# Kernel tuning notes

Measured on AMD Instinct MI355X. Metric: run time of the kernel, lower is better.

Reference implementation:

```python
import jax, jax.numpy as jnp
import numpy as np

B, DIM, H, W = 2, 256, 32, 32
HALF, DI, DS, DTR = DIM // 2, 256, 16, 8
DEPTH, K1 = 2, 4


def _ln(x, w, b, eps=1e-5):
    m = jnp.mean(x, -1, keepdims=True)
    v = jnp.var(x, -1, keepdims=True)
    return (x - m) * jax.lax.rsqrt(v + eps) * w + b


def _selective_scan(dA, dBu, C):
    # dA, dBu: (N, L, D, S); C: (N, L, S) -> y: (N, L, D)
    def step(h, ab):
        a, b = ab
        h = a * h + b
        return h, h
    h0 = jnp.zeros((dA.shape[0],) + dA.shape[2:], dA.dtype)
    _, hs = jax.lax.scan(step, h0, (jnp.moveaxis(dA, 1, 0), jnp.moveaxis(dBu, 1, 0)))
    return jnp.einsum('lnds,nls->nld', hs, C)


def _mamba_block(xs, ln_w, ln_b, in_w, cw, cb, xw, dtw, dtb, Alog, Dp, ow):
    # xs: (B, L, HALF); canonical Mamba-1 block, pre-LN residual
    Lq = xs.shape[1]
    h = _ln(xs, ln_w, ln_b)
    u, z = jnp.split(h @ in_w, 2, axis=-1)  # (B,L,DI) each
    up = jnp.pad(u, ((0, 0), (K1 - 1, 0), (0, 0)))  # causal depthwise conv1d
    u = sum(up[:, k:k + Lq, :] * cw[:, k] for k in range(K1)) + cb
    u = jax.nn.silu(u)
    dbc = u @ xw
    dtr, Bm, Cm = jnp.split(dbc, [DTR, DTR + DS], axis=-1)
    dt = jax.nn.softplus(dtr @ dtw + dtb)  # (B,L,DI)
    A = -jnp.exp(Alog)  # (DI,DS)
    dA = jnp.exp(dt[..., None] * A)
    dBu = (dt * u)[..., None] * Bm[:, :, None, :]
    y = _selective_scan(dA, dBu, Cm) + u * Dp
    return xs + (y * jax.nn.silu(z)) @ ow


def _vss_block(x, ln_w, ln_b, in_w, cw, cb, xw, dtw, dtb, Alog, Dp, on_w, on_b, ow):
    # x: (B, HALF, H, W); VMamba SS2D block (4-direction cross-scan), pre-LN residual
    Bq, _, Hq, Wq = x.shape
    Lq = Hq * Wq
    h = _ln(x.transpose(0, 2, 3, 1), ln_w, ln_b)
    u, z = jnp.split(h @ in_w, 2, axis=-1)  # (B,H,W,DI)
    u2 = jax.lax.conv_general_dilated(u.transpose(0, 3, 1, 2), cw[:, None], (1, 1), ((1, 1), (1, 1)),
                                      feature_group_count=DI,
                                      dimension_numbers=('NCHW', 'OIHW', 'NCHW')) + cb[None, :, None, None]
    u2 = jax.nn.silu(u2)  # (B,DI,H,W)
    s0 = u2.reshape(Bq, DI, Lq)
    s1 = u2.transpose(0, 1, 3, 2).reshape(Bq, DI, Lq)
    us = jnp.stack([s0, s1, jnp.flip(s0, -1), jnp.flip(s1, -1)], 1).transpose(0, 1, 3, 2)  # (B,4,L,DI)
    dbc = jnp.einsum('bkld,kdr->bklr', us, xw)
    dtr, Bm, Cm = jnp.split(dbc, [DTR, DTR + DS], axis=-1)
    dt = jax.nn.softplus(jnp.einsum('bklr,krd->bkld', dtr, dtw) + dtb[None, :, None, :])
    A = -jnp.exp(Alog)  # (4,DI,DS)
    dA = jnp.exp(dt[..., None] * A[None, :, None])  # (B,4,L,DI,DS)
    dBu = (dt * us)[..., None] * Bm[:, :, :, None, :]
    y = _selective_scan(dA.reshape(Bq * 4, Lq, DI, DS), dBu.reshape(Bq * 4, Lq, DI, DS), Cm.reshape(Bq * 4, Lq, DS))
    y = y.reshape(Bq, 4, Lq, DI) + us * Dp[None, :, None, :]
    yt = y.transpose(0, 1, 3, 2)  # (B,4,DI,L)
    y0 = yt[:, 0]
    y1 = yt[:, 1].reshape(Bq, DI, Wq, Hq).transpose(0, 1, 3, 2).reshape(Bq, DI, Lq)
    y2 = jnp.flip(yt[:, 2], -1)
    y3 = jnp.flip(yt[:, 3], -1).reshape(Bq, DI, Wq, Hq).transpose(0, 1, 3, 2).reshape(Bq, DI, Lq)
    ym = _ln((y0 + y1 + y2 + y3).transpose(0, 2, 1), on_w, on_b)  # (B,L,DI)
    out = (ym * jax.nn.silu(z.reshape(Bq, Lq, DI))) @ ow  # (B,L,HALF)
    return x + out.reshape(Bq, Hq, Wq, HALF).transpose(0, 3, 1, 2)


def _fwd(x, proj1_w, proj1_b, proj2_w, proj2_b,
         m_ln_w, m_ln_b, m_in_w, m_conv_w, m_conv_b, m_xproj_w, m_dt_w, m_dt_b, m_Alog, m_D, m_out_w,
         v_ln_w, v_ln_b, v_in_w, v_conv_w, v_conv_b, v_xproj_w, v_dt_w, v_dt_b, v_Alog, v_D,
         v_onorm_w, v_onorm_b, v_out_w, fuse_w, fuse_b, bn_g, bn_b, bn_m, bn_v):
    Bq, _, Hq, Wq = x.shape
    Lq = Hq * Wq
    p1 = jnp.einsum('oc,bchw->bohw', proj1_w, x) + proj1_b[None, :, None, None]
    s = p1.reshape(Bq, HALF, Lq).transpose(0, 2, 1)
    for i in range(DEPTH):
        s = _mamba_block(s, m_ln_w[i], m_ln_b[i], m_in_w[i], m_conv_w[i], m_conv_b[i], m_xproj_w[i],
                         m_dt_w[i], m_dt_b[i], m_Alog[i], m_D[i], m_out_w[i])
    p1 = s.transpose(0, 2, 1).reshape(Bq, HALF, Hq, Wq)
    p2 = jnp.einsum('oc,bchw->bohw', proj2_w, x) + proj2_b[None, :, None, None]
    for i in range(DEPTH):
        p2 = _vss_block(p2, v_ln_w[i], v_ln_b[i], v_in_w[i], v_conv_w[i], v_conv_b[i], v_xproj_w[i],
                        v_dt_w[i], v_dt_b[i], v_Alog[i], v_D[i], v_onorm_w[i], v_onorm_b[i], v_out_w[i])
    xc = jnp.concatenate([p1, p2], 1)
    y = jax.lax.conv_general_dilated(xc, fuse_w, (1, 1), ((1, 1), (1, 1)),
                                     dimension_numbers=('NCHW', 'OIHW', 'NCHW')) + fuse_b[None, :, None, None]
    y = (y - bn_m[None, :, None, None]) * jax.lax.rsqrt(bn_v + 1e-5)[None, :, None, None] * bn_g[None, :, None, None] + bn_b[None, :, None, None]
    return jax.nn.relu(y)


def setup_inputs() -> dict:
    key = jax.random.key(0)
    ks = iter(jax.random.split(key, 64))
    n = lambda shape, s=0.02: jax.random.normal(next(ks), shape, jnp.float32) * s
    A_row = jnp.log(jnp.arange(1, DS + 1, dtype=jnp.float32))  # standard S4D-real init
    return {
        'x': jax.random.normal(next(ks), (B, DIM, H, W), jnp.float32),
        'proj1_w': n((HALF, DIM), 0.05), 'proj1_b': n((HALF,)),
        'proj2_w': n((HALF, DIM), 0.05), 'proj2_b': n((HALF,)),
        'm_ln_w': jnp.ones((DEPTH, HALF)), 'm_ln_b': jnp.zeros((DEPTH, HALF)),
        'm_in_w': n((DEPTH, HALF, 2 * DI)),
        'm_conv_w': n((DEPTH, DI, K1), 0.1), 'm_conv_b': n((DEPTH, DI)),
        'm_xproj_w': n((DEPTH, DI, DTR + 2 * DS)),
        'm_dt_w': n((DEPTH, DTR, DI), 0.1), 'm_dt_b': n((DEPTH, DI)),
        'm_Alog': jnp.array(jnp.broadcast_to(A_row, (DEPTH, DI, DS))),
        'm_D': jnp.ones((DEPTH, DI)),
        'm_out_w': n((DEPTH, DI, HALF)),
        'v_ln_w': jnp.ones((DEPTH, HALF)), 'v_ln_b': jnp.zeros((DEPTH, HALF)),
        'v_in_w': n((DEPTH, HALF, 2 * DI)),
        'v_conv_w': n((DEPTH, DI, 3, 3), 0.1), 'v_conv_b': n((DEPTH, DI)),
        'v_xproj_w': n((DEPTH, 4, DI, DTR + 2 * DS)),
        'v_dt_w': n((DEPTH, 4, DTR, DI), 0.1), 'v_dt_b': n((DEPTH, 4, DI)),
        'v_Alog': jnp.array(jnp.broadcast_to(A_row, (DEPTH, 4, DI, DS))),
        'v_D': jnp.ones((DEPTH, 4, DI)),
        'v_onorm_w': jnp.ones((DEPTH, DI)), 'v_onorm_b': jnp.zeros((DEPTH, DI)),
        'v_out_w': n((DEPTH, DI, HALF)),
        'fuse_w': n((DIM, DIM, 3, 3), 0.02), 'fuse_b': n((DIM,)),
        'bn_g': jnp.ones((DIM,)), 'bn_b': jnp.zeros((DIM,)),
        'bn_m': n((DIM,)), 'bn_v': jax.random.uniform(next(ks), (DIM,), jnp.float32, 0.5, 1.5),
    }


def reference(x, proj1_w, proj1_b, proj2_w, proj2_b,
              m_ln_w, m_ln_b, m_in_w, m_conv_w, m_conv_b, m_xproj_w, m_dt_w, m_dt_b, m_Alog, m_D, m_out_w,
              v_ln_w, v_ln_b, v_in_w, v_conv_w, v_conv_b, v_xproj_w, v_dt_w, v_dt_b, v_Alog, v_D,
              v_onorm_w, v_onorm_b, v_out_w, fuse_w, fuse_b, bn_g, bn_b, bn_m, bn_v):
    return _fwd(x, proj1_w, proj1_b, proj2_w, proj2_b,
                m_ln_w, m_ln_b, m_in_w, m_conv_w, m_conv_b, m_xproj_w, m_dt_w, m_dt_b, m_Alog, m_D, m_out_w,
                v_ln_w, v_ln_b, v_in_w, v_conv_w, v_conv_b, v_xproj_w, v_dt_w, v_dt_b, v_Alog, v_D,
                v_onorm_w, v_onorm_b, v_out_w, fuse_w, fuse_b, bn_g, bn_b, bn_m, bn_v)
```

## Files before the change

kernel.cpp:

```cpp
#include <hip/hip_runtime.h>
#include <math.h>

#define CH  16
#define NCH 64

typedef __attribute__((ext_vector_type(8))) short bf16x8;
typedef __attribute__((ext_vector_type(4))) float f32x4;
typedef __attribute__((ext_vector_type(4))) unsigned int u32x4;

__device__ __forceinline__ float dev_silu(float x){ return x * (1.0f/(1.0f + __expf(-x))); }
__device__ __forceinline__ float dev_softplus(float x){ return fmaxf(x,0.0f) + log1pf(__expf(-fabsf(x))); }
__device__ __forceinline__ unsigned short dev_bf16(float f){
    unsigned int u = __float_as_uint(f);
    return (unsigned short)((u + 0x7fffu + ((u >> 16) & 1u)) >> 16);
}

__global__ void __launch_bounds__(256)
k_wt(const float* __restrict__ w1, const float* __restrict__ w2, float* __restrict__ wtc)
{
    int bc = blockIdx.x;
    int ot = bc & 7, ct = bc >> 3;
    __shared__ float t[32][33];
    int col = threadIdx.x & 31, r8 = threadIdx.x >> 5;
    #pragma unroll
    for (int i = 0; i < 4; ++i){
        int r = i*8 + r8;
        int o = ot*32 + r;
        const float* src = (o < 128) ? (w1 + (size_t)o*256) : (w2 + (size_t)(o-128)*256);
        t[r][col] = src[ct*32 + col];
    }
    __syncthreads();
    #pragma unroll
    for (int i = 0; i < 4; ++i){
        int r = i*8 + r8;
        int c = ct*32 + r, o = ot*32 + col;
        wtc[(size_t)c*256 + o] = t[col][r];
    }
}

__global__ void __launch_bounds__(256)
k_proj(const float* __restrict__ x, const float* __restrict__ wtc,
       const float* __restrict__ b1, const float* __restrict__ b2,
       float* __restrict__ sm, float* __restrict__ sv)
{
    int blk = blockIdx.x;
    int b = blk >> 8, l0 = (blk & 255) * 4;
    int tid = threadIdx.x;
    __shared__ float4 xs[256];
    xs[tid] = *(const float4*)(x + ((size_t)(b*256 + tid))*1024 + l0);
    __syncthreads();
    int o = tid & 127;
    float bias = (tid < 128) ? b1[o] : b2[o];
    float a0 = bias, a1 = bias, a2 = bias, a3 = bias;
    #pragma unroll 4
    for (int c = 0; c < 256; ++c){
        float wv = wtc[(size_t)c*256 + tid];
        float4 xv = xs[c];
        a0 = fmaf(wv, xv.x, a0);
        a1 = fmaf(wv, xv.y, a1);
        a2 = fmaf(wv, xv.z, a2);
        a3 = fmaf(wv, xv.w, a3);
    }
    float* dst = (tid < 128) ? sm : sv;
    size_t base = ((size_t)b*1024 + l0)*128 + o;
    dst[base      ] = a0;
    dst[base + 128] = a1;
    dst[base + 256] = a2;
    dst[base + 384] = a3;
}

__global__ void __launch_bounds__(256)
k_lnmm(const float* __restrict__ s, const float* __restrict__ lnw, const float* __restrict__ lnb,
       const float* __restrict__ inw, float* __restrict__ u, float* __restrict__ z)
{
    int bl0 = blockIdx.x * 8;
    int tid = threadIdx.x;
    int row = tid >> 5, lane = tid & 31;
    __shared__ float hn[8][132];
    float4 v = *(const float4*)(s + (size_t)(bl0 + row)*128 + lane*4);
    float a = v.x + v.y + v.z + v.w;
    float q = v.x*v.x + v.y*v.y + v.z*v.z + v.w*v.w;
    #pragma unroll
    for (int o = 16; o; o >>= 1){ a += __shfl_xor(a, o); q += __shfl_xor(q, o); }
    float mean = a * (1.0f/128.0f);
    float rs = rsqrtf(q * (1.0f/128.0f) - mean*mean + 1e-5f);
    float4 w4 = *(const float4*)(lnw + lane*4);
    float4 b4 = *(const float4*)(lnb + lane*4);
    float4 hv;
    hv.x = (v.x-mean)*rs*w4.x + b4.x;
    hv.y = (v.y-mean)*rs*w4.y + b4.y;
    hv.z = (v.z-mean)*rs*w4.z + b4.z;
    hv.w = (v.w-mean)*rs*w4.w + b4.w;
    *(float4*)&hn[row][lane*4] = hv;
    __syncthreads();
    float acc0[8] = {0,0,0,0,0,0,0,0};
    float acc1[8] = {0,0,0,0,0,0,0,0};
    for (int c = 0; c < 128; c += 4){
        float w0[4], w1[4];
        #pragma unroll
        for (int i = 0; i < 4; ++i){
            w0[i] = inw[(size_t)(c+i)*512 + tid];
            w1[i] = inw[(size_t)(c+i)*512 + tid + 256];
        }
        #pragma unroll
        for (int r = 0; r < 8; ++r){
            float4 h4 = *(const float4*)&hn[r][c];
            acc0[r] = fmaf(h4.x, w0[0], acc0[r]);
            acc0[r] = fmaf(h4.y, w0[1], acc0[r]);
            acc0[r] = fmaf(h4.z, w0[2], acc0[r]);
            acc0[r] = fmaf(h4.w, w0[3], acc0[r]);
            acc1[r] = fmaf(h4.x, w1[0], acc1[r]);
            acc1[r] = fmaf(h4.y, w1[1], acc1[r]);
            acc1[r] = fmaf(h4.z, w1[2], acc1[r]);
            acc1[r] = fmaf(h4.w, w1[3], acc1[r]);
        }
    }
    #pragma unroll
    for (int r = 0; r < 8; ++r){
        u[(size_t)(bl0 + r)*256 + tid] = acc0[r];
        z[(size_t)(bl0 + r)*256 + tid] = acc1[r];
    }
}

__global__ void __launch_bounds__(256)
k_mconv(const float* __restrict__ ur, const float* __restrict__ cw, const float* __restrict__ cb,
        float* __restrict__ uc)
{
    int bl = blockIdx.x; int b = bl >> 10, l = bl & 1023; int d = threadIdx.x;
    float acc = cb[d];
    #pragma unroll
    for (int k = 0; k < 4; ++k){
        int lp = l - 3 + k;
        if (lp >= 0) acc = fmaf(ur[((size_t)(b<<10) + lp)*256 + d], cw[d*4 + k], acc);
    }
    uc[(size_t)bl*256 + d] = dev_silu(acc);
}

__global__ void __launch_bounds__(256)
k_vconv(const float* __restrict__ ur, const float* __restrict__ cw, const float* __restrict__ cb,
        float* __restrict__ us)
{
    int bl = blockIdx.x; int b = bl >> 10, l = bl & 1023; int d = threadIdx.x;
    int h = l >> 5, w = l & 31;
    float acc = cb[d];
    #pragma unroll
    for (int kh = 0; kh < 3; ++kh){
        int hh = h + kh - 1; if (hh < 0 || hh > 31) continue;
        #pragma unroll
        for (int kw = 0; kw < 3; ++kw){
            int ww = w + kw - 1; if (ww < 0 || ww > 31) continue;
            acc = fmaf(ur[((size_t)(b<<10) + (hh<<5) + ww)*256 + d], cw[d*9 + kh*3 + kw], acc);
        }
    }
    float v = dev_silu(acc);
    int l1 = (w<<5) + h;
    size_t base = (size_t)b*4*1024*256;
    us[base + ((size_t)0*1024 + l        )*256 + d] = v;
    us[base + ((size_t)1*1024 + l1       )*256 + d] = v;
    us[base + ((size_t)2*1024 + (1023-l ))*256 + d] = v;
    us[base + ((size_t)3*1024 + (1023-l1))*256 + d] = v;
}

__global__ void __launch_bounds__(256)
k_xproj(const float* __restrict__ u, const float* __restrict__ xw, const float* __restrict__ dtw,
        const float* __restrict__ dtb, float* __restrict__ dt, float* __restrict__ Bm,
        float* __restrict__ Cm, int K)
{
    int blk = blockIdx.x;
    int bk = blk >> 8; int k = bk % K;
    int l0 = (blk & 255) * 4;
    size_t idx0 = (size_t)bk*1024 + l0;
    int tid = threadIdx.x;
    __shared__ float ursh[4][256];
    __shared__ float dbc[4][44];
    #pragma unroll
    for (int p = 0; p < 4; ++p)
        ursh[p][tid] = u[(idx0 + p)*256 + tid];
    __syncthreads();
    if (tid < 160){
        int r = tid % 40, p = tid / 40;
        const float* xwc = xw + (size_t)k*256*40 + r;
        float a0 = 0.f, a1 = 0.f;
        for (int c = 0; c < 128; ++c){
            a0 = fmaf(ursh[p][c],       xwc[(size_t)c*40],       a0);
            a1 = fmaf(ursh[p][c + 128], xwc[(size_t)(c+128)*40], a1);
        }
        dbc[p][r] = a0 + a1;
    }
    __syncthreads();
    const float* dtwk = dtw + (size_t)k*8*256;
    float bias = dtb[k*256 + tid];
    float wv[8];
    #pragma unroll
    for (int r = 0; r < 8; ++r) wv[r] = dtwk[r*256 + tid];
    #pragma unroll
    for (int p = 0; p < 4; ++p){
        float a = bias;
        #pragma unroll
        for (int r = 0; r < 8; ++r) a = fmaf(dbc[p][r], wv[r], a);
        dt[(idx0 + p)*256 + tid] = dev_softplus(a);
    }
    if (tid < 128){
        int p = tid >> 5, j = tid & 31;
        if (j < 16) Bm[(idx0 + p)*16 + j]        = dbc[p][8 + j];
        else        Cm[(idx0 + p)*16 + (j - 16)] = dbc[p][8 + j];
    }
}

__global__ void __launch_bounds__(256)
k_scanA(const float* __restrict__ dt, const float* __restrict__ u, const float* __restrict__ Bm,
        const float* __restrict__ Alog, float* __restrict__ Pb, float* __restrict__ Qb, int K)
{
    int blk = blockIdx.x;
    int c = blk & (NCH-1); int bk = blk >> 6; int k = bk % K;
    int d = threadIdx.x;
    __shared__ float Bsh[CH][16];
    {
        int j = threadIdx.x >> 4, s = threadIdx.x & 15;
        Bsh[j][s] = Bm[((size_t)bk*1024 + c*CH + j)*16 + s];
    }
    float dtv[CH], duv[CH];
    size_t base = ((size_t)bk*1024 + c*CH)*256 + d;
    #pragma unroll
    for (int j = 0; j < CH; ++j){
        float a = dt[base + (size_t)j*256];
        float b = u [base + (size_t)j*256];
        dtv[j] = a; duv[j] = a*b;
    }
    float A[16];
    const float4* Ap = (const float4*)(Alog + ((size_t)k*256 + d)*16);
    #pragma unroll
    for (int q = 0; q < 4; ++q){
        float4 v = Ap[q];
        A[q*4+0] = -__expf(v.x); A[q*4+1] = -__expf(v.y);
        A[q*4+2] = -__expf(v.z); A[q*4+3] = -__expf(v.w);
    }
    __syncthreads();
    float Q[16];
    #pragma unroll
    for (int s = 0; s < 16; ++s) Q[s] = 0.f;
    float S = 0.f;
    #pragma unroll
    for (int j = 0; j < CH; ++j){
        S += dtv[j];
        #pragma unroll
        for (int s = 0; s < 16; ++s){
            float av = __expf(dtv[j]*A[s]);
            Q[s] = fmaf(av, Q[s], duv[j]*Bsh[j][s]);
        }
    }
    float4* Pp = (float4*)(Pb + ((size_t)blk*256 + d)*16);
    float4* Qp = (float4*)(Qb + ((size_t)blk*256 + d)*16);
    #pragma unroll
    for (int q = 0; q < 4; ++q){
        float4 pv, qv;
        pv.x = __expf(S*A[q*4+0]); pv.y = __expf(S*A[q*4+1]);
        pv.z = __expf(S*A[q*4+2]); pv.w = __expf(S*A[q*4+3]);
        qv.x = Q[q*4+0]; qv.y = Q[q*4+1]; qv.z = Q[q*4+2]; qv.w = Q[q*4+3];
        Pp[q] = pv; Qp[q] = qv;
    }
}

__global__ void __launch_bounds__(256)
k_scanP(float* __restrict__ Pb, const float* __restrict__ Qb)
{
    int bk = blockIdx.x >> 4;
    int dg = blockIdx.x & 15;
    int tid = threadIdx.x;
    size_t idx0 = (size_t)bk*NCH*4096 + dg*256 + tid;
    float Pv[NCH], Qv[NCH];
    #pragma unroll
    for (int c = 0; c < NCH; ++c){
        Pv[c] = Pb[idx0 + (size_t)c*4096];
        Qv[c] = Qb[idx0 + (size_t)c*4096];
    }
    float h = 0.f;
    #pragma unroll
    for (int c = 0; c < NCH; ++c){
        Pb[idx0 + (size_t)c*4096] = h;
        h = fmaf(Pv[c], h, Qv[c]);
    }
}

__global__ void __launch_bounds__(256)
k_scanB(const float* __restrict__ dt, const float* __restrict__ u, const float* __restrict__ Bm,
        const float* __restrict__ Cm, const float* __restrict__ Alog,
        const float* __restrict__ Hb, float* __restrict__ y, int K)
{
    int blk = blockIdx.x;
    int c = blk & (NCH-1); int bk = blk >> 6; int k = bk % K;
    int d = threadIdx.x;
    __shared__ float Bsh[CH][16], Csh[CH][16];
    {
        int j = threadIdx.x >> 4, s = threadIdx.x & 15;
        size_t bi = ((size_t)bk*1024 + c*CH + j)*16 + s;
        Bsh[j][s] = Bm[bi];
        Csh[j][s] = Cm[bi];
    }
    float dtv[CH], duv[CH];
    size_t base = ((size_t)bk*1024 + c*CH)*256 + d;
    #pragma unroll
    for (int j = 0; j < CH; ++j){
        float a = dt[base + (size_t)j*256];
        float b = u [base + (size_t)j*256];
        dtv[j] = a; duv[j] = a*b;
    }
    float A[16];
    const float4* Ap = (const float4*)(Alog + ((size_t)k*256 + d)*16);
    #pragma unroll
    for (int q = 0; q < 4; ++q){
        float4 v = Ap[q];
        A[q*4+0] = -__expf(v.x); A[q*4+1] = -__expf(v.y);
        A[q*4+2] = -__expf(v.z); A[q*4+3] = -__expf(v.w);
    }
    float h[16];
    const float4* Hp = (const float4*)(Hb + ((size_t)blk*256 + d)*16);
    #pragma unroll
    for (int q = 0; q < 4; ++q){
        float4 v = Hp[q];
        h[q*4+0] = v.x; h[q*4+1] = v.y; h[q*4+2] = v.z; h[q*4+3] = v.w;
    }
    __syncthreads();
    float* yp = y + base;
    #pragma unroll
    for (int j = 0; j < CH; ++j){
        float py = 0.f;
        #pragma unroll
        for (int s = 0; s < 16; ++s){
            float av = __expf(dtv[j]*A[s]);
            h[s] = fmaf(av, h[s], duv[j]*Bsh[j][s]);
            py = fmaf(h[s], Csh[j][s], py);
        }
        yp[(size_t)j*256] = py;
    }
}

__global__ void __launch_bounds__(256)
k_mout(const float* __restrict__ y, const float* __restrict__ uc, const float* __restrict__ z,
       const float* __restrict__ Dp, const float* __restrict__ ow, float* __restrict__ sm)
{
    int bl0 = blockIdx.x * 8;
    int tid = threadIdx.x;
    int row = tid >> 5, c0 = (tid & 31) * 8;
    __shared__ float gld[8][264];
    size_t base = (size_t)(bl0 + row)*256 + c0;
    #pragma unroll
    for (int i = 0; i < 8; i += 4){
        float4 yv = *(const float4*)(y + base + i);
        float4 uv = *(const float4*)(uc + base + i);
        float4 zv = *(const float4*)(z + base + i);
        float4 dv = *(const float4*)(Dp + c0 + i);
        gld[row][c0+i+0] = (yv.x + uv.x*dv.x) * dev_silu(zv.x);
        gld[row][c0+i+1] = (yv.y + uv.y*dv.y) * dev_silu(zv.y);
        gld[row][c0+i+2] = (yv.z + uv.z*dv.z) * dev_silu(zv.z);
        gld[row][c0+i+3] = (yv.w + uv.w*dv.w) * dev_silu(zv.w);
    }
    __syncthreads();
    int o = tid & 127, rg = tid >> 7;
    float acc[4] = {0,0,0,0};
    for (int c = 0; c < 256; c += 4){
        float w[4];
        #pragma unroll
        for (int i = 0; i < 4; ++i) w[i] = ow[(size_t)(c+i)*128 + o];
        #pragma unroll
        for (int r = 0; r < 4; ++r){
            float4 h4 = *(const float4*)&gld[rg*4 + r][c];
            acc[r] = fmaf(h4.x, w[0], acc[r]);
            acc[r] = fmaf(h4.y, w[1], acc[r]);
            acc[r] = fmaf(h4.z, w[2], acc[r]);
            acc[r] = fmaf(h4.w, w[3], acc[r]);
        }
    }
    #pragma unroll
    for (int r = 0; r < 4; ++r)
        sm[(size_t)(bl0 + rg*4 + r)*128 + o] += acc[r];
}

__global__ void __launch_bounds__(256)
k_vcomb(const float* __restrict__ y, const float* __restrict__ us, const float* __restrict__ z,
        const float* __restrict__ Dp, const float* __restrict__ onw, const float* __restrict__ onb,
        const float* __restrict__ ow, float* __restrict__ sv)
{
    int blk = blockIdx.x;
    int b = blk >> 7;
    int l0 = (blk & 127) * 8;
    int tid = threadIdx.x;
    int row = tid >> 5, c0 = (tid & 31) * 8;
    int l = l0 + row;
    int h = l >> 5, w = l & 31;
    int l1 = (w<<5) + h, l2 = 1023 - l, l3 = 1023 - l1;
    size_t base = (size_t)b*4*1024*256;
    size_t i0 = base + ((size_t)0*1024 + l )*256 + c0;
    size_t i1 = base + ((size_t)1*1024 + l1)*256 + c0;
    size_t i2 = base + ((size_t)2*1024 + l2)*256 + c0;
    size_t i3 = base + ((size_t)3*1024 + l3)*256 + c0;
    float t[8];
    #pragma unroll
    for (int i = 0; i < 8; i += 4){
        float4 yv = *(const float4*)(y + i0 + i);
        float4 uv = *(const float4*)(us + i0 + i);
        float4 dv = *(const float4*)(Dp + 0*256 + c0 + i);
        t[i+0] = yv.x + uv.x*dv.x; t[i+1] = yv.y + uv.y*dv.y;
        t[i+2] = yv.z + uv.z*dv.z; t[i+3] = yv.w + uv.w*dv.w;
    }
    #pragma unroll
    for (int i = 0; i < 8; i += 4){
        float4 yv = *(const float4*)(y + i1 + i);
        float4 uv = *(const float4*)(us + i1 + i);
        float4 dv = *(const float4*)(Dp + 1*256 + c0 + i);
        t[i+0] += yv.x + uv.x*dv.x; t[i+1] += yv.y + uv.y*dv.y;
        t[i+2] += yv.z + uv.z*dv.z; t[i+3] += yv.w + uv.w*dv.w;
    }
    #pragma unroll
    for (int i = 0; i < 8; i += 4){
        float4 yv = *(const float4*)(y + i2 + i);
        float4 uv = *(const float4*)(us + i2 + i);
        float4 dv = *(const float4*)(Dp + 2*256 + c0 + i);
        t[i+0] += yv.x + uv.x*dv.x; t[i+1] += yv.y + uv.y*dv.y;
        t[i+2] += yv.z + uv.z*dv.z; t[i+3] += yv.w + uv.w*dv.w;
    }
    #pragma unroll
    for (int i = 0; i < 8; i += 4){
        float4 yv = *(const float4*)(y + i3 + i);
        float4 uv = *(const float4*)(us + i3 + i);
        float4 dv = *(const float4*)(Dp + 3*256 + c0 + i);
        t[i+0] += yv.x + uv.x*dv.x; t[i+1] += yv.y + uv.y*dv.y;
        t[i+2] += yv.z + uv.z*dv.z; t[i+3] += yv.w + uv.w*dv.w;
    }
    float a = 0.f, q = 0.f;
    #pragma unroll
    for (int i = 0; i < 8; ++i){ a += t[i]; q += t[i]*t[i]; }
    #pragma unroll
    for (int o = 16; o; o >>= 1){ a += __shfl_xor(a, o); q += __shfl_xor(q, o); }
    float mean = a * (1.0f/256.0f);
    float rs = rsqrtf(q * (1.0f/256.0f) - mean*mean + 1e-5f);
    __shared__ float gld[8][264];
    size_t zbase = (size_t)(b*1024 + l)*256 + c0;
    #pragma unroll
    for (int i = 0; i < 8; i += 4){
        float4 wv = *(const float4*)(onw + c0 + i);
        float4 bv = *(const float4*)(onb + c0 + i);
        float4 zv = *(const float4*)(z + zbase + i);
        gld[row][c0+i+0] = ((t[i+0]-mean)*rs*wv.x + bv.x) * dev_silu(zv.x);
        gld[row][c0+i+1] = ((t[i+1]-mean)*rs*wv.y + bv.y) * dev_silu(zv.y);
        gld[row][c0+i+2] = ((t[i+2]-mean)*rs*wv.z + bv.z) * dev_silu(zv.z);
        gld[row][c0+i+3] = ((t[i+3]-mean)*rs*wv.w + bv.w) * dev_silu(zv.w);
    }
    __syncthreads();
    int o = tid & 127, rg = tid >> 7;
    float acc[4] = {0,0,0,0};
    for (int c = 0; c < 256; c += 4){
        float wv[4];
        #pragma unroll
        for (int i = 0; i < 4; ++i) wv[i] = ow[(size_t)(c+i)*128 + o];
        #pragma unroll
        for (int r = 0; r < 4; ++r){
            float4 h4 = *(const float4*)&gld[rg*4 + r][c];
            acc[r] = fmaf(h4.x, wv[0], acc[r]);
            acc[r] = fmaf(h4.y, wv[1], acc[r]);
            acc[r] = fmaf(h4.z, wv[2], acc[r]);
            acc[r] = fmaf(h4.w, wv[3], acc[r]);
        }
    }
    #pragma unroll
    for (int r = 0; r < 4; ++r)
        sv[(size_t)(b*1024 + l0 + rg*4 + r)*128 + o] += acc[r];
}

__global__ void __launch_bounds__(256)
k_wconv(const float* __restrict__ fw, unsigned short* __restrict__ Wb)
{
    int idx = (blockIdx.x*256 + threadIdx.x)*4;
    float4 v = *(const float4*)(fw + idx);
    unsigned int r0 = dev_bf16(v.x), r1 = dev_bf16(v.y), r2 = dev_bf16(v.z), r3 = dev_bf16(v.w);
    uint2 pk; pk.x = r0 | (r1 << 16); pk.y = r2 | (r3 << 16);
    *(uint2*)(Wb + idx) = pk;
}

__global__ void __launch_bounds__(256)
k_im2col(const float* __restrict__ sm, const float* __restrict__ sv,
         unsigned short* __restrict__ Bt)
{
    int n = blockIdx.x; int b = n >> 10, p = n & 1023;
    int h = p >> 5, w = p & 31;
    int tid = threadIdx.x;
    #pragma unroll
    for (int it = 0; it < 9; ++it){
        int k = it*256 + tid;
        int c = k / 9, r = k - c*9;
        int kh = r / 3, kw = r - kh*3;
        int hh = h + kh - 1, ww = w + kw - 1;
        float v = 0.f;
        if (hh >= 0 && hh < 32 && ww >= 0 && ww < 32){
            int l = (hh << 5) + ww;
            v = (c < 128) ? sm[((size_t)b*1024 + l)*128 + c]
                          : sv[((size_t)b*1024 + l)*128 + (c - 128)];
        }
        Bt[(size_t)n*2304 + k] = dev_bf16(v);
    }
}

__global__ void __launch_bounds__(256)
k_fgemm(const unsigned short* __restrict__ Wb, const unsigned short* __restrict__ Bt,
        const float* __restrict__ fb, const float* __restrict__ bg, const float* __restrict__ bb,
        const float* __restrict__ bm, const float* __restrict__ bv, float* __restrict__ out)
{
    int o0 = (blockIdx.x & 3) * 64;
    int n0 = (blockIdx.x >> 2) * 64;
    int tid = threadIdx.x, lane = tid & 63, wid = tid >> 6;
    int wm = (wid >> 1) * 32, wn = (wid & 1) * 32;
    __shared__ unsigned short sA[64*40];
    __shared__ unsigned short sB[64*40];
    f32x4 acc[2][2] = {};
    int srow = tid >> 2, scol = (tid & 3) * 8;
    const u32x4* gA = (const u32x4*)(Wb + (size_t)(o0 + srow)*2304 + scol);
    const u32x4* gB = (const u32x4*)(Bt + (size_t)(n0 + srow)*2304 + scol);
    u32x4* wA = (u32x4*)(sA + srow*40 + scol);
    u32x4* wB = (u32x4*)(sB + srow*40 + scol);
    int fr = lane & 15, fk = (lane >> 4) * 8;
    const unsigned short* rA0 = sA + (wm + fr)*40 + fk;
    const unsigned short* rA1 = sA + (wm + 16 + fr)*40 + fk;
    const unsigned short* rB0 = sB + (wn + fr)*40 + fk;
    const unsigned short* rB1 = sB + (wn + 16 + fr)*40 + fk;
    for (int kt = 0; kt < 72; ++kt){
        u32x4 va = gA[kt*4];
        u32x4 vb = gB[kt*4];
        __syncthreads();
        *wA = va; *wB = vb;
        __syncthreads();
        bf16x8 a0 = *(const bf16x8*)rA0;
        bf16x8 a1 = *(const bf16x8*)rA1;
        bf16x8 b0 = *(const bf16x8*)rB0;
        bf16x8 b1 = *(const bf16x8*)rB1;
        acc[0][0] = __builtin_amdgcn_mfma_f32_16x16x32_bf16(a0, b0, acc[0][0], 0, 0, 0);
        acc[0][1] = __builtin_amdgcn_mfma_f32_16x16x32_bf16(a0, b1, acc[0][1], 0, 0, 0);
        acc[1][0] = __builtin_amdgcn_mfma_f32_16x16x32_bf16(a1, b0, acc[1][0], 0, 0, 0);
        acc[1][1] = __builtin_amdgcn_mfma_f32_16x16x32_bf16(a1, b1, acc[1][1], 0, 0, 0);
    }
    #pragma unroll
    for (int i = 0; i < 2; ++i){
        int ob = o0 + wm + i*16 + (lane >> 4) * 4;
        #pragma unroll
        for (int j = 0; j < 2; ++j){
            int n = n0 + wn + j*16 + (lane & 15);
            int b = n >> 10, p = n & 1023;
            #pragma unroll
            for (int q = 0; q < 4; ++q){
                int o = ob + q;
                float v = acc[i][j][q] + fb[o];
                v = (v - bm[o]) * rsqrtf(bv[o] + 1e-5f) * bg[o] + bb[o];
                out[((size_t)(b*256 + o))*1024 + p] = fmaxf(v, 0.f);
            }
        }
    }
}

extern "C" void kernel_launch(void* const* d_in, const int* in_sizes, int n_in,
                              void* d_out, int out_size, void* d_ws, size_t ws_size,
                              hipStream_t stream)
{
    const float* x         = (const float*)d_in[0];
    const float* proj1_w   = (const float*)d_in[1];
    const float* proj1_b   = (const float*)d_in[2];
    const float* proj2_w   = (const float*)d_in[3];
    const float* proj2_b   = (const float*)d_in[4];
    const float* m_ln_w    = (const float*)d_in[5];
    const float* m_ln_b    = (const float*)d_in[6];
    const float* m_in_w    = (const float*)d_in[7];
    const float* m_conv_w  = (const float*)d_in[8];
    const float* m_conv_b  = (const float*)d_in[9];
    const float* m_xproj_w = (const float*)d_in[10];
    const float* m_dt_w    = (const float*)d_in[11];
    const float* m_dt_b    = (const float*)d_in[12];
    const float* m_Alog    = (const float*)d_in[13];
    const float* m_D       = (const float*)d_in[14];
    const float* m_out_w   = (const float*)d_in[15];
    const float* v_ln_w    = (const float*)d_in[16];
    const float* v_ln_b    = (const float*)d_in[17];
    const float* v_in_w    = (const float*)d_in[18];
    const float* v_conv_w  = (const float*)d_in[19];
    const float* v_conv_b  = (const float*)d_in[20];
    const float* v_xproj_w = (const float*)d_in[21];
    const float* v_dt_w    = (const float*)d_in[22];
    const float* v_dt_b    = (const float*)d_in[23];
    const float* v_Alog    = (const float*)d_in[24];
    const float* v_D       = (const float*)d_in[25];
    const float* v_onorm_w = (const float*)d_in[26];
    const float* v_onorm_b = (const float*)d_in[27];
    const float* v_out_w   = (const float*)d_in[28];
    const float* fuse_w    = (const float*)d_in[29];
    const float* fuse_b    = (const float*)d_in[30];
    const float* bn_g      = (const float*)d_in[31];
    const float* bn_b      = (const float*)d_in[32];
    const float* bn_m      = (const float*)d_in[33];
    const float* bn_v      = (const float*)d_in[34];
    float* out = (float*)d_out;

    float* ws = (float*)d_ws;
    float* sm    = ws;  ws += 2*1024*128;
    float* sv    = ws;  ws += 2*1024*128;
    float* uraw  = ws;  ws += 2*1024*256;
    float* zb    = ws;  ws += 2*1024*256;
    float* uc    = ws;  ws += 2*1024*256;
    float* usb   = ws;  ws += 2*4*1024*256;
    float* dtb_  = ws;  ws += 2*4*1024*256;
    float* yb    = ws;  ws += 2*4*1024*256;
    float* Pb    = ws;  ws += 2*4*NCH*256*16;
    float* Qb    = ws;  ws += 2*4*NCH*256*16;
    float* Bmb   = ws;  ws += 2*4*1024*16;
    float* Cmb   = ws;  ws += 2*4*1024*16;
    float* wtc   = ws;  ws += 256*256;
    unsigned short* Wbf   = (unsigned short*)uraw;
    unsigned short* Bmat  = (unsigned short*)dtb_;

    k_wt  <<<64,    256, 0, stream>>>(proj1_w, proj2_w, wtc);
    k_proj<<<2*256, 256, 0, stream>>>(x, wtc, proj1_b, proj2_b, sm, sv);

    for (int i = 0; i < 2; ++i){
        k_lnmm <<<256,    256, 0, stream>>>(sm, m_ln_w + i*128, m_ln_b + i*128,
                                            m_in_w + (size_t)i*128*512, uraw, zb);
        k_mconv<<<2*1024, 256, 0, stream>>>(uraw, m_conv_w + (size_t)i*256*4, m_conv_b + i*256, uc);
        k_xproj<<<2*256,  256, 0, stream>>>(uc, m_xproj_w + (size_t)i*256*40,
                                            m_dt_w + (size_t)i*8*256, m_dt_b + i*256,
                                            dtb_, Bmb, Cmb, 1);
        k_scanA<<<2*NCH, 256, 0, stream>>>(dtb_, uc, Bmb, m_Alog + (size_t)i*256*16, Pb, Qb, 1);
        k_scanP<<<2*16,  256, 0, stream>>>(Pb, Qb);
        k_scanB<<<2*NCH, 256, 0, stream>>>(dtb_, uc, Bmb, Cmb, m_Alog + (size_t)i*256*16,
                                           Pb, yb, 1);
        k_mout <<<256,   256, 0, stream>>>(yb, uc, zb, m_D + i*256,
                                           m_out_w + (size_t)i*256*128, sm);
    }

    for (int i = 0; i < 2; ++i){
        k_lnmm <<<256,      256, 0, stream>>>(sv, v_ln_w + i*128, v_ln_b + i*128,
                                              v_in_w + (size_t)i*128*512, uraw, zb);
        k_vconv<<<2*1024,   256, 0, stream>>>(uraw, v_conv_w + (size_t)i*256*9, v_conv_b + i*256, usb);
        k_xproj<<<2*4*256,  256, 0, stream>>>(usb, v_xproj_w + (size_t)i*4*256*40,
                                              v_dt_w + (size_t)i*4*8*256, v_dt_b + (size_t)i*4*256,
                                              dtb_, Bmb, Cmb, 4);
        k_scanA<<<2*4*NCH, 256, 0, stream>>>(dtb_, usb, Bmb, v_Alog + (size_t)i*4*256*16,
                                             Pb, Qb, 4);
        k_scanP<<<2*4*16,  256, 0, stream>>>(Pb, Qb);
        k_scanB<<<2*4*NCH, 256, 0, stream>>>(dtb_, usb, Bmb, Cmb, v_Alog + (size_t)i*4*256*16,
                                             Pb, yb, 4);
        k_vcomb<<<256,      256, 0, stream>>>(yb, usb, zb, v_D + (size_t)i*4*256,
                                              v_onorm_w + i*256, v_onorm_b + i*256,
                                              v_out_w + (size_t)i*256*128, sv);
    }

    k_wconv <<<576,     256, 0, stream>>>(fuse_w, Wbf);
    k_im2col<<<2*1024,  256, 0, stream>>>(sm, sv, Bmat);
    k_fgemm <<<4*32,    256, 0, stream>>>(Wbf, Bmat, fuse_b, bn_g, bn_b, bn_m, bn_v, out);
}
```

Before: 362.6 us.

## Batch Mamba and VSS branches into shared launches per layer

```diff
diff --git a/kernel.cpp b/kernel.cpp
--- a/kernel.cpp
+++ b/kernel.cpp
@@ -16,25 +16,34 @@
 }
 
 __global__ void __launch_bounds__(256)
-k_wt(const float* __restrict__ w1, const float* __restrict__ w2, float* __restrict__ wtc)
-{
-    int bc = blockIdx.x;
-    int ot = bc & 7, ct = bc >> 3;
-    __shared__ float t[32][33];
-    int col = threadIdx.x & 31, r8 = threadIdx.x >> 5;
-    #pragma unroll
-    for (int i = 0; i < 4; ++i){
-        int r = i*8 + r8;
-        int o = ot*32 + r;
-        const float* src = (o < 128) ? (w1 + (size_t)o*256) : (w2 + (size_t)(o-128)*256);
-        t[r][col] = src[ct*32 + col];
-    }
-    __syncthreads();
-    #pragma unroll
-    for (int i = 0; i < 4; ++i){
-        int r = i*8 + r8;
-        int c = ct*32 + r, o = ot*32 + col;
-        wtc[(size_t)c*256 + o] = t[col][r];
+k_prep(const float* __restrict__ w1, const float* __restrict__ w2, float* __restrict__ wtc,
+       const float* __restrict__ fw, unsigned short* __restrict__ Wb)
+{
+    if (blockIdx.x < 64){
+        int bc = blockIdx.x;
+        int ot = bc & 7, ct = bc >> 3;
+        __shared__ float t[32][33];
+        int col = threadIdx.x & 31, r8 = threadIdx.x >> 5;
+        #pragma unroll
+        for (int i = 0; i < 4; ++i){
+            int r = i*8 + r8;
+            int o = ot*32 + r;
+            const float* src = (o < 128) ? (w1 + (size_t)o*256) : (w2 + (size_t)(o-128)*256);
+            t[r][col] = src[ct*32 + col];
+        }
+        __syncthreads();
+        #pragma unroll
+        for (int i = 0; i < 4; ++i){
+            int r = i*8 + r8;
+            int c = ct*32 + r, o = ot*32 + col;
+            wtc[(size_t)c*256 + o] = t[col][r];
+        }
+    } else {
+        int idx = ((blockIdx.x - 64)*256 + threadIdx.x)*4;
+        float4 v = *(const float4*)(fw + idx);
+        unsigned int r0 = dev_bf16(v.x), r1 = dev_bf16(v.y), r2 = dev_bf16(v.z), r3 = dev_bf16(v.w);
+        uint2 pk; pk.x = r0 | (r1 << 16); pk.y = r2 | (r3 << 16);
+        *(uint2*)(Wb + idx) = pk;
     }
 }
 
@@ -69,11 +78,10 @@
     dst[base + 384] = a3;
 }
 
-__global__ void __launch_bounds__(256)
-k_lnmm(const float* __restrict__ s, const float* __restrict__ lnw, const float* __restrict__ lnb,
-       const float* __restrict__ inw, float* __restrict__ u, float* __restrict__ z)
-{
-    int bl0 = blockIdx.x * 8;
+__device__ __forceinline__ void lnmm_body(int bl0, const float* __restrict__ s,
+    const float* __restrict__ lnw, const float* __restrict__ lnb,
+    const float* __restrict__ inw, float* __restrict__ u, float* __restrict__ z)
+{
     int tid = threadIdx.x;
     int row = tid >> 5, lane = tid & 31;
     __shared__ float hn[8][132];
@@ -123,53 +131,58 @@
 }
 
 __global__ void __launch_bounds__(256)
-k_mconv(const float* __restrict__ ur, const float* __restrict__ cw, const float* __restrict__ cb,
-        float* __restrict__ uc)
-{
-    int bl = blockIdx.x; int b = bl >> 10, l = bl & 1023; int d = threadIdx.x;
-    float acc = cb[d];
-    #pragma unroll
-    for (int k = 0; k < 4; ++k){
-        int lp = l - 3 + k;
-        if (lp >= 0) acc = fmaf(ur[((size_t)(b<<10) + lp)*256 + d], cw[d*4 + k], acc);
-    }
-    uc[(size_t)bl*256 + d] = dev_silu(acc);
-}
-
-__global__ void __launch_bounds__(256)
-k_vconv(const float* __restrict__ ur, const float* __restrict__ cw, const float* __restrict__ cb,
+k_lnmm2(const float* __restrict__ sm_, const float* __restrict__ mlnw, const float* __restrict__ mlnb,
+        const float* __restrict__ minw, float* __restrict__ um, float* __restrict__ zm,
+        const float* __restrict__ sv_, const float* __restrict__ vlnw, const float* __restrict__ vlnb,
+        const float* __restrict__ vinw, float* __restrict__ uv, float* __restrict__ zv)
+{
+    if (blockIdx.x < 256) lnmm_body(blockIdx.x*8, sm_, mlnw, mlnb, minw, um, zm);
+    else                  lnmm_body((blockIdx.x-256)*8, sv_, vlnw, vlnb, vinw, uv, zv);
+}
+
+__global__ void __launch_bounds__(256)
+k_conv2(const float* __restrict__ urm, const float* __restrict__ cwm, const float* __restrict__ cbm,
+        float* __restrict__ uc,
+        const float* __restrict__ urv, const float* __restrict__ cwv, const float* __restrict__ cbv,
         float* __restrict__ us)
 {
-    int bl = blockIdx.x; int b = bl >> 10, l = bl & 1023; int d = threadIdx.x;
-    int h = l >> 5, w = l & 31;
-    float acc = cb[d];
-    #pragma unroll
-    for (int kh = 0; kh < 3; ++kh){
-        int hh = h + kh - 1; if (hh < 0 || hh > 31) continue;
-        #pragma unroll
-        for (int kw = 0; kw < 3; ++kw){
-            int ww = w + kw - 1; if (ww < 0 || ww > 31) continue;
-            acc = fmaf(ur[((size_t)(b<<10) + (hh<<5) + ww)*256 + d], cw[d*9 + kh*3 + kw], acc);
-        }
-    }
-    float v = dev_silu(acc);
-    int l1 = (w<<5) + h;
-    size_t base = (size_t)b*4*1024*256;
-    us[base + ((size_t)0*1024 + l        )*256 + d] = v;
-    us[base + ((size_t)1*1024 + l1       )*256 + d] = v;
-    us[base + ((size_t)2*1024 + (1023-l ))*256 + d] = v;
-    us[base + ((size_t)3*1024 + (1023-l1))*256 + d] = v;
-}
-
-__global__ void __launch_bounds__(256)
-k_xproj(const float* __restrict__ u, const float* __restrict__ xw, const float* __restrict__ dtw,
-        const float* __restrict__ dtb, float* __restrict__ dt, float* __restrict__ Bm,
-        float* __restrict__ Cm, int K)
-{
-    int blk = blockIdx.x;
-    int bk = blk >> 8; int k = bk % K;
-    int l0 = (blk & 255) * 4;
-    size_t idx0 = (size_t)bk*1024 + l0;
+    int d = threadIdx.x;
+    if (blockIdx.x < 2048){
+        int bl = blockIdx.x; int b = bl >> 10, l = bl & 1023;
+        float acc = cbm[d];
+        #pragma unroll
+        for (int k = 0; k < 4; ++k){
+            int lp = l - 3 + k;
+            if (lp >= 0) acc = fmaf(urm[((size_t)(b<<10) + lp)*256 + d], cwm[d*4 + k], acc);
+        }
+        uc[(size_t)bl*256 + d] = dev_silu(acc);
+    } else {
+        int bl = blockIdx.x - 2048; int b = bl >> 10, l = bl & 1023;
+        int h = l >> 5, w = l & 31;
+        float acc = cbv[d];
+        #pragma unroll
+        for (int kh = 0; kh < 3; ++kh){
+            int hh = h + kh - 1; if (hh < 0 || hh > 31) continue;
+            #pragma unroll
+            for (int kw = 0; kw < 3; ++kw){
+                int ww = w + kw - 1; if (ww < 0 || ww > 31) continue;
+                acc = fmaf(urv[((size_t)(b<<10) + (hh<<5) + ww)*256 + d], cwv[d*9 + kh*3 + kw], acc);
+            }
+        }
+        float v = dev_silu(acc);
+        int l1 = (w<<5) + h;
+        size_t base = (size_t)b*4*1024*256;
+        us[base + ((size_t)0*1024 + l        )*256 + d] = v;
+        us[base + ((size_t)1*1024 + l1       )*256 + d] = v;
+        us[base + ((size_t)2*1024 + (1023-l ))*256 + d] = v;
+        us[base + ((size_t)3*1024 + (1023-l1))*256 + d] = v;
+    }
+}
+
+__device__ __forceinline__ void xproj_body(size_t idx0, int k, const float* __restrict__ u,
+    const float* __restrict__ xw, const float* __restrict__ dtw, const float* __restrict__ dtb,
+    float* __restrict__ dt, float* __restrict__ Bm, float* __restrict__ Cm)
+{
     int tid = threadIdx.x;
     __shared__ float ursh[4][256];
     __shared__ float dbc[4][44];
@@ -208,11 +221,29 @@
 }
 
 __global__ void __launch_bounds__(256)
-k_scanA(const float* __restrict__ dt, const float* __restrict__ u, const float* __restrict__ Bm,
-        const float* __restrict__ Alog, float* __restrict__ Pb, float* __restrict__ Qb, int K)
-{
-    int blk = blockIdx.x;
-    int c = blk & (NCH-1); int bk = blk >> 6; int k = bk % K;
+k_xproj2(const float* __restrict__ um, const float* __restrict__ mxw, const float* __restrict__ mdtw,
+         const float* __restrict__ mdtb, float* __restrict__ dtm, float* __restrict__ Bmm,
+         float* __restrict__ Cmm,
+         const float* __restrict__ uv, const float* __restrict__ vxw, const float* __restrict__ vdtw,
+         const float* __restrict__ vdtb, float* __restrict__ dtv, float* __restrict__ Bmv,
+         float* __restrict__ Cmv)
+{
+    if (blockIdx.x < 512){
+        int bk = blockIdx.x >> 8;
+        size_t idx0 = (size_t)bk*1024 + (blockIdx.x & 255)*4;
+        xproj_body(idx0, 0, um, mxw, mdtw, mdtb, dtm, Bmm, Cmm);
+    } else {
+        int blk = blockIdx.x - 512;
+        int bk = blk >> 8;
+        size_t idx0 = (size_t)bk*1024 + (blk & 255)*4;
+        xproj_body(idx0, bk & 3, uv, vxw, vdtw, vdtb, dtv, Bmv, Cmv);
+    }
+}
+
+__device__ __forceinline__ void scanA_body(int bk, int c, int k, const float* __restrict__ dt,
+    const float* __restrict__ u, const float* __restrict__ Bm, const float* __restrict__ Alog,
+    float* __restrict__ Pb, float* __restrict__ Qb)
+{
     int d = threadIdx.x;
     __shared__ float Bsh[CH][16];
     {
@@ -249,8 +280,9 @@
             Q[s] = fmaf(av, Q[s], duv[j]*Bsh[j][s]);
         }
     }
-    float4* Pp = (float4*)(Pb + ((size_t)blk*256 + d)*16);
-    float4* Qp = (float4*)(Qb + ((size_t)blk*256 + d)*16);
+    size_t oidx = ((size_t)(bk*NCH + c)*256 + d)*16;
+    float4* Pp = (float4*)(Pb + oidx);
+    float4* Qp = (float4*)(Qb + oidx);
     #pragma unroll
     for (int q = 0; q < 4; ++q){
         float4 pv, qv;
@@ -262,10 +294,24 @@
 }
 
 __global__ void __launch_bounds__(256)
-k_scanP(float* __restrict__ Pb, const float* __restrict__ Qb)
-{
-    int bk = blockIdx.x >> 4;
-    int dg = blockIdx.x & 15;
+k_scanA2(const float* __restrict__ dtm, const float* __restrict__ um, const float* __restrict__ Bmm,
+         const float* __restrict__ mAlog, float* __restrict__ Pbm, float* __restrict__ Qbm,
+         const float* __restrict__ dtv, const float* __restrict__ uv, const float* __restrict__ Bmv,
+         const float* __restrict__ vAlog, float* __restrict__ Pbv, float* __restrict__ Qbv)
+{
+    if (blockIdx.x < 128){
+        int blk = blockIdx.x;
+        scanA_body(blk >> 6, blk & (NCH-1), 0, dtm, um, Bmm, mAlog, Pbm, Qbm);
+    } else {
+        int blk = blockIdx.x - 128;
+        int bk = blk >> 6;
+        scanA_body(bk, blk & (NCH-1), bk & 3, dtv, uv, Bmv, vAlog, Pbv, Qbv);
+    }
+}
+
+__device__ __forceinline__ void scanP_body(int bk, int dg, float* __restrict__ Pb,
+                                           const float* __restrict__ Qb)
+{
     int tid = threadIdx.x;
     size_t idx0 = (size_t)bk*NCH*4096 + dg*256 + tid;
     float Pv[NCH], Qv[NCH];
@@ -283,12 +329,17 @@
 }
 
 __global__ void __launch_bounds__(256)
-k_scanB(const float* __restrict__ dt, const float* __restrict__ u, const float* __restrict__ Bm,
-        const float* __restrict__ Cm, const float* __restrict__ Alog,
-        const float* __restrict__ Hb, float* __restrict__ y, int K)
-{
-    int blk = blockIdx.x;
-    int c = blk & (NCH-1); int bk = blk >> 6; int k = bk % K;
+k_scanP2(float* __restrict__ Pbm, const float* __restrict__ Qbm,
+         float* __restrict__ Pbv, const float* __restrict__ Qbv)
+{
+    if (blockIdx.x < 32) scanP_body(blockIdx.x >> 4, blockIdx.x & 15, Pbm, Qbm);
+    else { int blk = blockIdx.x - 32; scanP_body(blk >> 4, blk & 15, Pbv, Qbv); }
+}
+
+__device__ __forceinline__ void scanB_body(int bk, int c, int k, const float* __restrict__ dt,
+    const float* __restrict__ u, const float* __restrict__ Bm, const float* __restrict__ Cm,
+    const float* __restrict__ Alog, const float* __restrict__ Hb, float* __restrict__ y)
+{
     int d = threadIdx.x;
     __shared__ float Bsh[CH][16], Csh[CH][16];
     {
@@ -314,7 +365,7 @@
         A[q*4+2] = -__expf(v.z); A[q*4+3] = -__expf(v.w);
     }
     float h[16];
-    const float4* Hp = (const float4*)(Hb + ((size_t)blk*256 + d)*16);
+    const float4* Hp = (const float4*)(Hb + ((size_t)(bk*NCH + c)*256 + d)*16);
     #pragma unroll
     for (int q = 0; q < 4; ++q){
         float4 v = Hp[q];
@@ -336,10 +387,27 @@
 }
 
 __global__ void __launch_bounds__(256)
-k_mout(const float* __restrict__ y, const float* __restrict__ uc, const float* __restrict__ z,
-       const float* __restrict__ Dp, const float* __restrict__ ow, float* __restrict__ sm)
-{
-    int bl0 = blockIdx.x * 8;
+k_scanB2(const float* __restrict__ dtm, const float* __restrict__ um, const float* __restrict__ Bmm,
+         const float* __restrict__ Cmm, const float* __restrict__ mAlog,
+         const float* __restrict__ Hbm, float* __restrict__ ym,
+         const float* __restrict__ dtv, const float* __restrict__ uv, const float* __restrict__ Bmv,
+         const float* __restrict__ Cmv, const float* __restrict__ vAlog,
+         const float* __restrict__ Hbv, float* __restrict__ yv)
+{
+    if (blockIdx.x < 128){
+        int blk = blockIdx.x;
+        scanB_body(blk >> 6, blk & (NCH-1), 0, dtm, um, Bmm, Cmm, mAlog, Hbm, ym);
+    } else {
+        int blk = blockIdx.x - 128;
+        int bk = blk >> 6;
+        scanB_body(bk, blk & (NCH-1), bk & 3, dtv, uv, Bmv, Cmv, vAlog, Hbv, yv);
+    }
+}
+
+__device__ __forceinline__ void mout_body(int bl0, const float* __restrict__ y,
+    const float* __restrict__ uc, const float* __restrict__ z, const float* __restrict__ Dp,
+    const float* __restrict__ ow, float* __restrict__ sm)
+{
     int tid = threadIdx.x;
     int row = tid >> 5, c0 = (tid & 31) * 8;
     __shared__ float gld[8][264];
@@ -376,12 +444,11 @@
         sm[(size_t)(bl0 + rg*4 + r)*128 + o] += acc[r];
 }
 
-__global__ void __launch_bounds__(256)
-k_vcomb(const float* __restrict__ y, const float* __restrict__ us, const float* __restrict__ z,
-        const float* __restrict__ Dp, const float* __restrict__ onw, const float* __restrict__ onb,
-        const float* __restrict__ ow, float* __restrict__ sv)
-{
-    int blk = blockIdx.x;
+__device__ __forceinline__ void vcomb_body(int blk, const float* __restrict__ y,
+    const float* __restrict__ us, const float* __restrict__ z, const float* __restrict__ Dp,
+    const float* __restrict__ onw, const float* __restrict__ onb, const float* __restrict__ ow,
+    float* __restrict__ sv)
+{
     int b = blk >> 7;
     int l0 = (blk & 127) * 8;
     int tid = threadIdx.x;
@@ -468,13 +535,14 @@
 }
 
 __global__ void __launch_bounds__(256)
-k_wconv(const float* __restrict__ fw, unsigned short* __restrict__ Wb)
-{
-    int idx = (blockIdx.x*256 + threadIdx.x)*4;
-    float4 v = *(const float4*)(fw + idx);
-    unsigned int r0 = dev_bf16(v.x), r1 = dev_bf16(v.y), r2 = dev_bf16(v.z), r3 = dev_bf16(v.w);
-    uint2 pk; pk.x = r0 | (r1 << 16); pk.y = r2 | (r3 << 16);
-    *(uint2*)(Wb + idx) = pk;
+k_epi2(const float* __restrict__ ym, const float* __restrict__ uc, const float* __restrict__ zm,
+       const float* __restrict__ mD, const float* __restrict__ mow, float* __restrict__ sm,
+       const float* __restrict__ yv, const float* __restrict__ us, const float* __restrict__ zv,
+       const float* __restrict__ vD, const float* __restrict__ onw, const float* __restrict__ onb,
+       const float* __restrict__ vow, float* __restrict__ sv)
+{
+    if (blockIdx.x < 256) mout_body(blockIdx.x*8, ym, uc, zm, mD, mow, sm);
+    else                  vcomb_body(blockIdx.x-256, yv, us, zv, vD, onw, onb, vow, sv);
 }
 
 __global__ void __launch_bounds__(256)
@@ -597,58 +665,60 @@
     float* out = (float*)d_out;
 
     float* ws = (float*)d_ws;
-    float* sm    = ws;  ws += 2*1024*128;
-    float* sv    = ws;  ws += 2*1024*128;
-    float* uraw  = ws;  ws += 2*1024*256;
-    float* zb    = ws;  ws += 2*1024*256;
-    float* uc    = ws;  ws += 2*1024*256;
-    float* usb   = ws;  ws += 2*4*1024*256;
-    float* dtb_  = ws;  ws += 2*4*1024*256;
-    float* yb    = ws;  ws += 2*4*1024*256;
-    float* Pb    = ws;  ws += 2*4*NCH*256*16;
-    float* Qb    = ws;  ws += 2*4*NCH*256*16;
-    float* Bmb   = ws;  ws += 2*4*1024*16;
-    float* Cmb   = ws;  ws += 2*4*1024*16;
-    float* wtc   = ws;  ws += 256*256;
-    unsigned short* Wbf   = (unsigned short*)uraw;
-    unsigned short* Bmat  = (unsigned short*)dtb_;
-
-    k_wt  <<<64,    256, 0, stream>>>(proj1_w, proj2_w, wtc);
+    float* sm     = ws;  ws += 2*1024*128;
+    float* sv     = ws;  ws += 2*1024*128;
+    float* uraw_m = ws;  ws += 2*1024*256;
+    float* zb_m   = ws;  ws += 2*1024*256;
+    float* uc     = ws;  ws += 2*1024*256;
+    float* uraw_v = ws;  ws += 2*1024*256;
+    float* zb_v   = ws;  ws += 2*1024*256;
+    float* usb    = ws;  ws += 2*4*1024*256;
+    float* dt_m   = ws;  ws += 2*1024*256;
+    float* yb_m   = ws;  ws += 2*1024*256;
+    float* Pb_m   = ws;  ws += 2*NCH*256*16;
+    float* Qb_m   = ws;  ws += 2*NCH*256*16;
+    float* Bm_m   = ws;  ws += 2*1024*16;
+    float* Cm_m   = ws;  ws += 2*1024*16;
+    float* dt_v   = ws;  ws += 2*4*1024*256;
+    float* yb_v   = ws;  ws += 2*4*1024*256;
+    float* Pb_v   = ws;  ws += 2*4*NCH*256*16;
+    float* Qb_v   = ws;  ws += 2*4*NCH*256*16;
+    float* Bm_v   = ws;  ws += 2*4*1024*16;
+    float* Cm_v   = ws;  ws += 2*4*1024*16;
+    float* wtc    = ws;  ws += 256*256;
+    unsigned short* Wbf = (unsigned short*)ws;  ws += 576*1024/2;
+    unsigned short* Bmat = (unsigned short*)dt_v;
+
+    k_prep<<<640,   256, 0, stream>>>(proj1_w, proj2_w, wtc, fuse_w, Wbf);
     k_proj<<<2*256, 256, 0, stream>>>(x, wtc, proj1_b, proj2_b, sm, sv);
 
     for (int i = 0; i < 2; ++i){
-        k_lnmm <<<256,    256, 0, stream>>>(sm, m_ln_w + i*128, m_ln_b + i*128,
-                                            m_in_w + (size_t)i*128*512, uraw, zb);
-        k_mconv<<<2*1024, 256, 0, stream>>>(uraw, m_conv_w + (size_t)i*256*4, m_conv_b + i*256, uc);
-        k_xproj<<<2*256,  256, 0, stream>>>(uc, m_xproj_w + (size_t)i*256*40,
-                                            m_dt_w + (size_t)i*8*256, m_dt_b + i*256,
-                                            dtb_, Bmb, Cmb, 1);
-        k_scanA<<<2*NCH, 256, 0, stream>>>(dtb_, uc, Bmb, m_Alog + (size_t)i*256*16, Pb, Qb, 1);
-        k_scanP<<<2*16,  256, 0, stream>>>(Pb, Qb);
-        k_scanB<<<2*NCH, 256, 0, stream>>>(dtb_, uc, Bmb, Cmb, m_Alog + (size_t)i*256*16,
-                                           Pb, yb, 1);
-        k_mout <<<256,   256, 0, stream>>>(yb, uc, zb, m_D + i*256,
-                                           m_out_w + (size_t)i*256*128, sm);
-    }
-
-    for (int i = 0; i < 2; ++i){
-        k_lnmm <<<256,      256, 0, stream>>>(sv, v_ln_w + i*128, v_ln_b + i*128,
-                                              v_in_w + (size_t)i*128*512, uraw, zb);
-        k_vconv<<<2*1024,   256, 0, stream>>>(uraw, v_conv_w + (size_t)i*256*9, v_conv_b + i*256, usb);
-        k_xproj<<<2*4*256,  256, 0, stream>>>(usb, v_xproj_w + (size_t)i*4*256*40,
-                                              v_dt_w + (size_t)i*4*8*256, v_dt_b + (size_t)i*4*256,
-                                              dtb_, Bmb, Cmb, 4);
-        k_scanA<<<2*4*NCH, 256, 0, stream>>>(dtb_, usb, Bmb, v_Alog + (size_t)i*4*256*16,
-                                             Pb, Qb, 4);
-        k_scanP<<<2*4*16,  256, 0, stream>>>(Pb, Qb);
-        k_scanB<<<2*4*NCH, 256, 0, stream>>>(dtb_, usb, Bmb, Cmb, v_Alog + (size_t)i*4*256*16,
-                                             Pb, yb, 4);
-        k_vcomb<<<256,      256, 0, stream>>>(yb, usb, zb, v_D + (size_t)i*4*256,
-                                              v_onorm_w + i*256, v_onorm_b + i*256,
-                                              v_out_w + (size_t)i*256*128, sv);
-    }
-
-    k_wconv <<<576,     256, 0, stream>>>(fuse_w, Wbf);
-    k_im2col<<<2*1024,  256, 0, stream>>>(sm, sv, Bmat);
-    k_fgemm <<<4*32,    256, 0, stream>>>(Wbf, Bmat, fuse_b, bn_g, bn_b, bn_m, bn_v, out);
-}
+        k_lnmm2 <<<512,  256, 0, stream>>>(sm, m_ln_w + i*128, m_ln_b + i*128,
+                                           m_in_w + (size_t)i*65536, uraw_m, zb_m,
+                                           sv, v_ln_w + i*128, v_ln_b + i*128,
+                                           v_in_w + (size_t)i*65536, uraw_v, zb_v);
+        k_conv2 <<<4096, 256, 0, stream>>>(uraw_m, m_conv_w + (size_t)i*1024, m_conv_b + i*256, uc,
+                                           uraw_v, v_conv_w + (size_t)i*2304, v_conv_b + i*256, usb);
+        k_xproj2<<<2560, 256, 0, stream>>>(uc,  m_xproj_w + (size_t)i*10240,
+                                           m_dt_w + (size_t)i*2048, m_dt_b + i*256,
+                                           dt_m, Bm_m, Cm_m,
+                                           usb, v_xproj_w + (size_t)i*40960,
+                                           v_dt_w + (size_t)i*8192, v_dt_b + (size_t)i*1024,
+                                           dt_v, Bm_v, Cm_v);
+        k_scanA2<<<640,  256, 0, stream>>>(dt_m, uc,  Bm_m, m_Alog + (size_t)i*4096,  Pb_m, Qb_m,
+                                           dt_v, usb, Bm_v, v_Alog + (size_t)i*16384, Pb_v, Qb_v);
+        k_scanP2<<<160,  256, 0, stream>>>(Pb_m, Qb_m, Pb_v, Qb_v);
+        k_scanB2<<<640,  256, 0, stream>>>(dt_m, uc,  Bm_m, Cm_m, m_Alog + (size_t)i*4096,
+                                           Pb_m, yb_m,
+                                           dt_v, usb, Bm_v, Cm_v, v_Alog + (size_t)i*16384,
+                                           Pb_v, yb_v);
+        k_epi2  <<<512,  256, 0, stream>>>(yb_m, uc, zb_m, m_D + i*256,
+                                           m_out_w + (size_t)i*32768, sm,
+                                           yb_v, usb, zb_v, v_D + (size_t)i*1024,
+                                           v_onorm_w + i*256, v_onorm_b + i*256,
+                                           v_out_w + (size_t)i*32768, sv);
+    }
+
+    k_im2col<<<2*1024, 256, 0, stream>>>(sm, sv, Bmat);
+    k_fgemm <<<4*32,   256, 0, stream>>>(Wbf, Bmat, fuse_b, bn_g, bn_b, bn_m, bn_v, out);
+}
```

New measurement: 297.1 us. -18.1%, faster.
